# Performance work log

Hardware: AMD Instinct MI355X
Metric: run time of the kernel (lower is better)

Reference implementation:

```python
import jax, jax.numpy as jnp
import numpy as np

B, T, H, V = 32, 16, 768, 32000
EPS = 1e-5


def _conv(x, w, stride, pad):
    return jax.lax.conv_general_dilated(
        x, w, (stride, stride), [(pad, pad), (pad, pad)],
        dimension_numbers=('NCHW', 'OIHW', 'NCHW'))


def _bn(x, g, b, m, v):
    inv = g / jnp.sqrt(v + EPS)
    return x * inv[None, :, None, None] + (b - m * inv)[None, :, None, None]


def setup_inputs() -> dict:
    key = jax.random.key(0)
    ks = iter(jax.random.split(key, 48))

    def rn(shape, s=0.02):
        return s * jax.random.normal(next(ks), shape, jnp.float32)

    def bn_params(c):
        g = 1.0 + 0.1 * jax.random.normal(next(ks), (c,), jnp.float32)
        b = 0.1 * jax.random.normal(next(ks), (c,), jnp.float32)
        m = 0.1 * jax.random.normal(next(ks), (c,), jnp.float32)
        v = jax.random.uniform(next(ks), (c,), jnp.float32, 0.5, 1.5)
        return g, b, m, v

    inp = {}
    inp['images'] = jax.random.normal(next(ks), (B, 3, 224, 224), jnp.float32)
    inp['captions'] = jax.random.randint(next(ks), (B, T), 0, V)

    inp['conv1_w'] = rn((64, 3, 7, 7))
    inp['bn1_g'], inp['bn1_b'], inp['bn1_m'], inp['bn1_v'] = bn_params(64)
    inp['conv2_w'] = rn((128, 64, 3, 3))
    inp['bn2_g'], inp['bn2_b'], inp['bn2_m'], inp['bn2_v'] = bn_params(128)
    inp['conv3_w'] = rn((256, 128, 3, 3))
    inp['bn3_g'], inp['bn3_b'], inp['bn3_m'], inp['bn3_v'] = bn_params(256)
    inp['conv4_w'] = rn((H, 256, 3, 3))
    inp['bn4_g'], inp['bn4_b'], inp['bn4_m'], inp['bn4_v'] = bn_params(H)

    emb = rn((V, H), 1.0)
    inp['emb_table'] = emb.at[0].set(0.0)  # padding_idx=0 row is zero
    inp['attn_w'] = rn((H, H))             # attn_proj (no bias)
    inp['w_ih'] = rn((4 * H, 2 * H))       # LSTM input weights (i,f,g,o)
    inp['w_hh'] = rn((4 * H, H))
    inp['b_ih'] = rn((4 * H,))
    inp['b_hh'] = rn((4 * H,))
    inp['fc_w'] = rn((V, H))
    inp['fc_b'] = rn((V,))
    return inp


def _forward(images, captions, conv1_w, bn1_g, bn1_b, bn1_m, bn1_v,
             conv2_w, bn2_g, bn2_b, bn2_m, bn2_v,
             conv3_w, bn3_g, bn3_b, bn3_m, bn3_v,
             conv4_w, bn4_g, bn4_b, bn4_m, bn4_v,
             emb_table, attn_w, w_ih, w_hh, b_ih, b_hh, fc_w, fc_b):
    # ---- ResNetEncoder ----
    x = jax.nn.relu(_bn(_conv(images, conv1_w, 2, 3), bn1_g, bn1_b, bn1_m, bn1_v))
    x = jax.lax.reduce_window(x, -jnp.inf, jax.lax.max, (1, 1, 3, 3), (1, 1, 2, 2),
                              ((0, 0), (0, 0), (1, 1), (1, 1)))
    x = jax.nn.relu(_bn(_conv(x, conv2_w, 1, 1), bn2_g, bn2_b, bn2_m, bn2_v))
    x = jax.nn.relu(_bn(_conv(x, conv3_w, 2, 1), bn3_g, bn3_b, bn3_m, bn3_v))
    x = jax.nn.relu(_bn(_conv(x, conv4_w, 1, 1), bn4_g, bn4_b, bn4_m, bn4_v))
    b, c, hh, ww = x.shape
    memory = x.reshape(b, c, hh * ww).transpose(0, 2, 1)[:, :196, :]  # [B,196,H]

    # ---- LSTMAttnDecoder ----
    emb = emb_table[captions]  # [B,T,H]
    h0 = jnp.zeros((b, H), jnp.float32)
    c0 = jnp.zeros((b, H), jnp.float32)

    def step(carry, e_t):
        h, cst = carry
        q = h @ attn_w.T                                    # [B,H]
        scores = jnp.einsum('bh,bmh->bm', q, memory)        # [B,196]
        ctx = jnp.einsum('bm,bmh->bh', jax.nn.softmax(scores, axis=-1), memory)
        xin = jnp.concatenate([e_t, ctx], axis=-1)          # [B,2H]
        gates = xin @ w_ih.T + b_ih + h @ w_hh.T + b_hh     # [B,4H]
        i, f, g, o = jnp.split(gates, 4, axis=-1)
        c_new = jax.nn.sigmoid(f) * cst + jax.nn.sigmoid(i) * jnp.tanh(g)
        h_new = jax.nn.sigmoid(o) * jnp.tanh(c_new)
        logits = h_new @ fc_w.T + fc_b                      # [B,V]
        return (h_new, c_new), logits

    (hT, cT), logits = jax.lax.scan(step, (h0, c0), emb.transpose(1, 0, 2))
    logits = logits.transpose(1, 0, 2)  # [B,T,V]
    return logits, (hT[None], cT[None])


def reference(images, captions, conv1_w, bn1_g, bn1_b, bn1_m, bn1_v,
              conv2_w, bn2_g, bn2_b, bn2_m, bn2_v,
              conv3_w, bn3_g, bn3_b, bn3_m, bn3_v,
              conv4_w, bn4_g, bn4_b, bn4_m, bn4_v,
              emb_table, attn_w, w_ih, w_hh, b_ih, b_hh, fc_w, fc_b):
    return _forward(images, captions, conv1_w, bn1_g, bn1_b, bn1_m, bn1_v,
                    conv2_w, bn2_g, bn2_b, bn2_m, bn2_v,
                    conv3_w, bn3_g, bn3_b, bn3_m, bn3_v,
                    conv4_w, bn4_g, bn4_b, bn4_m, bn4_v,
                    emb_table, attn_w, w_ih, w_hh, b_ih, b_hh, fc_w, fc_b)
```

## Files before the change

### kernel.cpp

```cpp
#include <hip/hip_runtime.h>
#include <math.h>

#define NB 32
#define NT 16
#define NH 768
#define NV 32000

typedef short bf16x8 __attribute__((ext_vector_type(8)));
typedef float floatx4 __attribute__((ext_vector_type(4)));
typedef unsigned short ushort_t;

__device__ __forceinline__ float bf2f(unsigned short h) {
    unsigned u = ((unsigned)h) << 16;
    return __builtin_bit_cast(float, u);
}
__device__ __forceinline__ unsigned short f2bf(float f) {
    unsigned u = __builtin_bit_cast(unsigned, f);
    u += 0x7fffu + ((u >> 16) & 1u);
    return (unsigned short)(u >> 16);
}
__device__ __forceinline__ float sigmoidf_(float x) { return 1.f / (1.f + expf(-x)); }

__device__ __forceinline__ int swz8(int bid, int N) {
    return (bid & 7) * (N >> 3) + (bid >> 3);
}

__device__ __forceinline__ bf16x8 cvt8(float4 a, float4 b) {
    bf16x8 t;
    t[0] = (short)f2bf(a.x); t[1] = (short)f2bf(a.y);
    t[2] = (short)f2bf(a.z); t[3] = (short)f2bf(a.w);
    t[4] = (short)f2bf(b.x); t[5] = (short)f2bf(b.y);
    t[6] = (short)f2bf(b.z); t[7] = (short)f2bf(b.w);
    return t;
}

#define SEG0 1216
#define SEG1 (SEG0 + 10240)
#define SEG2 (SEG1 + 73728)
#define SEG3 (SEG2 + 294912)
#define SEG4 (SEG3 + 1769472)
#define SEG5 (SEG4 + 589824)
#define SEG6 (SEG5 + 4718592)
#define SEG7 (SEG6 + 294912)
#define SEG8 (SEG7 + 393216)
#define SEG9 (SEG8 + 49152)
__global__ __launch_bounds__(256) void prep_all(
    const float* __restrict__ g1, const float* __restrict__ b1, const float* __restrict__ m1, const float* __restrict__ v1,
    const float* __restrict__ g2, const float* __restrict__ b2, const float* __restrict__ m2, const float* __restrict__ v2,
    const float* __restrict__ g3, const float* __restrict__ b3, const float* __restrict__ m3, const float* __restrict__ v3,
    const float* __restrict__ g4, const float* __restrict__ b4, const float* __restrict__ m4, const float* __restrict__ v4,
    float* __restrict__ s1, float* __restrict__ o1, float* __restrict__ s2, float* __restrict__ o2,
    float* __restrict__ s3, float* __restrict__ o3, float* __restrict__ s4, float* __restrict__ o4,
    const float* __restrict__ conv1_w, ushort_t* __restrict__ wb1,
    const float* __restrict__ conv2_w, ushort_t* __restrict__ wb2,
    const float* __restrict__ conv3_w, ushort_t* __restrict__ wb3,
    const float* __restrict__ conv4_w, ushort_t* __restrict__ wb4,
    const float* __restrict__ attn_w, ushort_t* __restrict__ wattnTP,
    const float* __restrict__ w_ih, const float* __restrict__ w_hh, ushort_t* __restrict__ wcombP,
    ushort_t* __restrict__ wihL,
    const int* __restrict__ caps, const float* __restrict__ table, ushort_t* __restrict__ e512P,
    float* __restrict__ hbuf, float* __restrict__ cbuf, ushort_t* __restrict__ xinA,
    unsigned long long* __restrict__ halo, long long n8) {
    long long gi = (long long)blockIdx.x * 256 + threadIdx.x;
    if (gi < SEG0) {
        int i = (int)gi;
        const float *g, *b, *m, *v;
        float *s, *o;
        int c;
        if (i < 64)        { g = g1; b = b1; m = m1; v = v1; s = s1; o = o1; c = i; }
        else if (i < 192)  { g = g2; b = b2; m = m2; v = v2; s = s2; o = o2; c = i - 64; }
        else if (i < 448)  { g = g3; b = b3; m = m3; v = v3; s = s3; o = o3; c = i - 192; }
        else               { g = g4; b = b4; m = m4; v = v4; s = s4; o = o4; c = i - 448; }
        float inv = g[c] * rsqrtf(v[c] + 1e-5f);
        s[c] = inv;
        o[c] = b[c] - m[c] * inv;
    } else if (gi < SEG1) {
        int idx = (int)(gi - SEG0);
        int co = idx / 160, k = idx % 160;
        wb1[idx] = (k < 147) ? f2bf(conv1_w[co * 147 + k]) : (ushort_t)0;
    } else if (gi < SEG4) {
        const float* w;
        ushort_t* dst;
        int CIN, idx;
        if (gi < SEG2)      { w = conv2_w; dst = wb2; CIN = 64;  idx = (int)(gi - SEG1); }
        else if (gi < SEG3) { w = conv3_w; dst = wb3; CIN = 128; idx = (int)(gi - SEG2); }
        else                { w = conv4_w; dst = wb4; CIN = 256; idx = (int)(gi - SEG3); }
        int e = idx & 7, lane = (idx >> 3) & 63, j = (idx >> 9) & 3;
        int r = idx >> 11;
        int KQ = CIN >> 5;
        int kq = r % KQ; r /= KQ;
        int tap = r % 9; int nt = r / 9;
        int co = nt * 64 + j * 16 + (lane & 15);
        int ci = kq * 32 + (lane >> 4) * 8 + e;
        dst[idx] = f2bf(w[((size_t)co * CIN + ci) * 9 + tap]);
    } else if (gi < SEG5) {
        int idx = (int)(gi - SEG4);
        int e = idx & 7, lane = (idx >> 3) & 63, j = (idx >> 9) & 3;
        int t = idx >> 11;
        int kq = t % 24, nt = t / 24;
        int n = nt * 64 + 16 * j + (lane & 15);
        int k = kq * 32 + (lane >> 4) * 8 + e;
        wattnTP[idx] = f2bf(attn_w[(size_t)k * 768 + n]);
    } else if (gi < SEG6) {
        int idx = (int)(gi - SEG5);
        int e = idx & 7, lane = (idx >> 3) & 63;
        int t = idx >> 9;
        int kq = t % 48, gg = t / 48;
        int g = gg & 3, bx = gg >> 2;
        int j = g * 768 + bx * 16 + (lane & 15);
        int k = kq * 32 + (lane >> 4) * 8 + e;
        float v = (k < NH) ? w_ih[(size_t)j * (2 * NH) + NH + k] : w_hh[(size_t)j * NH + (k - NH)];
        wcombP[idx] = f2bf(v);
    } else if (gi < SEG7) {
        int idx = (int)(gi - SEG6);
        int r = idx / 96, g = idx % 96;
        const float4* s = (const float4*)(w_ih + (size_t)r * 1536 + g * 8);
        *(bf16x8*)(wihL + (size_t)idx * 8) = cvt8(s[0], s[1]);
    } else if (gi < SEG8) {
        int idx = (int)(gi - SEG7);
        int e = idx & 7, lane = (idx >> 3) & 63, i = (idx >> 9) & 3;
        int t2 = idx >> 11;
        int kq = t2 % 24, mt = t2 / 24;
        int r = mt * 64 + i * 16 + (lane & 15);
        int k = kq * 32 + (lane >> 4) * 8 + e;
        int t = r >> 5, b = r & 31;
        e512P[idx] = f2bf(table[(size_t)caps[b * NT + t] * NH + k]);
    } else if (gi < SEG9) {
        int i = (int)(gi - SEG8);
        xinA[i] = 0;
        if (i < NB * NH) { hbuf[i] = 0.f; cbuf[i] = 0.f; }
    } else {
        long long j = gi - SEG9;
        if (j < n8) halo[j] = 0ULL;
    }
}

__global__ __launch_bounds__(256) void im2col1(const float* __restrict__ img, ushort_t* __restrict__ A) {
    int idx = blockIdx.x * 256 + threadIdx.x;
    const int total = 121856 * 160;
    if (idx >= total) return;
    int k = idx % 160;
    int m = idx / 160;
    ushort_t v = 0;
    if (k < 147) {
        int b = m / 3808;
        int rm = m % 3808;
        int y = rm / 112, x = rm % 112;
        int ci = k / 49;
        int r = k % 49;
        int ky = r / 7, kx = r % 7;
        int iy = 2 * y - 3 + ky;
        int ix = 2 * x - 3 + kx;
        if ((unsigned)iy < 224u && (unsigned)ix < 224u)
            v = f2bf(img[((size_t)(b * 3 + ci) * 224 + iy) * 224 + ix]);
    }
    A[idx] = v;
}

__global__ __launch_bounds__(256) void cvt_b16rows(const float* __restrict__ src, ushort_t* __restrict__ dst,
                                                   int cols8, int ldsrc, int total8) {
    int i = blockIdx.x * 256 + threadIdx.x;
    if (i >= total8) return;
    int r = i / cols8, g = i % cols8;
    const float4* s = (const float4*)(src + (size_t)r * ldsrc + g * 8);
    *(bf16x8*)(dst + (size_t)i * 8) = cvt8(s[0], s[1]);
}

__global__ __launch_bounds__(256) void conv1_gemm(
    const ushort_t* __restrict__ A, const ushort_t* __restrict__ Bw,
    const float* __restrict__ scale, const float* __restrict__ bias,
    ushort_t* __restrict__ out) {
    int lane = threadIdx.x & 63, w = threadIdx.x >> 6;
    int m0 = (blockIdx.x * 4 + w) * 64;
    int lr = lane & 15, kl = (lane >> 4) * 8;
    floatx4 acc[4][4];
    #pragma unroll
    for (int i = 0; i < 4; ++i)
        #pragma unroll
        for (int j = 0; j < 4; ++j) acc[i][j] = 0.f;
    #pragma unroll
    for (int k0 = 0; k0 < 160; k0 += 32) {
        bf16x8 a[4], bb[4];
        #pragma unroll
        for (int i = 0; i < 4; ++i) a[i] = *(const bf16x8*)(A + (size_t)(m0 + 16 * i + lr) * 160 + kl + k0);
        #pragma unroll
        for (int j = 0; j < 4; ++j) bb[j] = *(const bf16x8*)(Bw + (size_t)(16 * j + lr) * 160 + kl + k0);
        #pragma unroll
        for (int i = 0; i < 4; ++i)
            #pragma unroll
            for (int j = 0; j < 4; ++j)
                acc[i][j] = __builtin_amdgcn_mfma_f32_16x16x32_bf16(a[i], bb[j], acc[i][j], 0, 0, 0);
    }
    #pragma unroll
    for (int i = 0; i < 4; ++i) {
        #pragma unroll
        for (int r = 0; r < 4; ++r) {
            int m = m0 + 16 * i + (lane >> 4) * 4 + r;
            int b = m / 3808;
            int rm = m % 3808;
            int y = rm / 112, x = rm % 112;
            #pragma unroll
            for (int j = 0; j < 4; ++j) {
                int n = 16 * j + lr;
                float v = fmaxf(acc[i][j][r] * scale[n] + bias[n], 0.f);
                out[((size_t)(b * 34 + y) * 112 + x) * 64 + n] = f2bf(v);
            }
        }
    }
}

__global__ __launch_bounds__(256) void pool_kernel(const ushort_t* __restrict__ in,
                                                   ushort_t* __restrict__ hal2) {
    int idx = blockIdx.x * 256 + threadIdx.x;
    const int total = 32 * 17 * 56 * 8;
    if (idx >= total) return;
    int c8 = idx & 7;
    int rest = idx >> 3;
    int x = rest % 56; rest /= 56;
    int y = rest % 17; int b = rest / 17;
    float mx[8];
    #pragma unroll
    for (int j = 0; j < 8; ++j) mx[j] = -INFINITY;
    for (int dy = -1; dy <= 1; ++dy) {
        int iy = 2 * y + dy;
        if ((unsigned)iy >= 34u) continue;
        for (int dx = -1; dx <= 1; ++dx) {
            int ix = 2 * x + dx;
            if ((unsigned)ix >= 112u) continue;
            bf16x8 v = *(const bf16x8*)(in + (((size_t)(b * 34 + iy)) * 112 + ix) * 64 + c8 * 8);
            #pragma unroll
            for (int j = 0; j < 8; ++j) mx[j] = fmaxf(mx[j], bf2f((unsigned short)v[j]));
        }
    }
    bf16x8 o;
    #pragma unroll
    for (int j = 0; j < 8; ++j) o[j] = (short)f2bf(mx[j]);
    *(bf16x8*)(hal2 + (((size_t)(b * 19 + y + 1)) * 58 + (x + 1)) * 64 + c8 * 8) = o;
}

template <int CIN, int HH, int WH, int STRIDE, int HOUT, int WOUT, int COUT, int OH, int OW>
__global__ __launch_bounds__(64) void conv_mfma(
    const ushort_t* __restrict__ in, const ushort_t* __restrict__ wtP,
    const float* __restrict__ scale, const float* __restrict__ bias,
    ushort_t* __restrict__ out) {
    const int KQ = CIN / 32;
    const int NK = 9 * KQ;
    const int MT = (32 * HOUT * WOUT) / 64;
    const int NTL = COUT / 64;
    int id = swz8(blockIdx.x, MT * NTL);
    int mt = id % MT, nt = id / MT;
    int lane = threadIdx.x;
    int lr = lane & 15, kl = (lane >> 4) * 8;
    int rowoff[4];
    #pragma unroll
    for (int i = 0; i < 4; ++i) {
        int m = mt * 64 + 16 * i + lr;
        int b = m / (HOUT * WOUT);
        int rm = m % (HOUT * WOUT);
        int y = rm / WOUT, x = rm % WOUT;
        rowoff[i] = ((b * HH + y * STRIDE) * WH + x * STRIDE) * CIN + kl;
    }
    floatx4 acc[4][4];
    #pragma unroll
    for (int i = 0; i < 4; ++i)
        #pragma unroll
        for (int j = 0; j < 4; ++j) acc[i][j] = 0.f;

    auto ioffOf = [&](int ks) {
        int tap = ks / KQ;
        int k0 = (ks & (KQ - 1)) * 32;
        int ky = tap / 3, kx = tap - ky * 3;
        return (ky * WH + kx) * CIN + k0;
    };
    const ushort_t* bbase = wtP + ((size_t)nt * 9 * KQ * 4 * 64 + lane) * 8;

    bf16x8 aC[4], bC[4], aN[4], bN[4];
    {
        int io = ioffOf(0);
        #pragma unroll
        for (int i = 0; i < 4; ++i) aC[i] = *(const bf16x8*)(in + rowoff[i] + io);
        #pragma unroll
        for (int j = 0; j < 4; ++j) bC[j] = *(const bf16x8*)(bbase + ((size_t)j * 64) * 8);
    }
    for (int ks = 0; ks < NK; ks += 2) {
        {
            int io = ioffOf(ks + 1);
            #pragma unroll
            for (int i = 0; i < 4; ++i) aN[i] = *(const bf16x8*)(in + rowoff[i] + io);
            #pragma unroll
            for (int j = 0; j < 4; ++j) bN[j] = *(const bf16x8*)(bbase + ((size_t)((ks + 1) * 4 + j) * 64) * 8);
        }
        #pragma unroll
        for (int i = 0; i < 4; ++i)
            #pragma unroll
            for (int j = 0; j < 4; ++j)
                acc[i][j] = __builtin_amdgcn_mfma_f32_16x16x32_bf16(aC[i], bC[j], acc[i][j], 0, 0, 0);
        if (ks + 2 < NK) {
            int io = ioffOf(ks + 2);
            #pragma unroll
            for (int i = 0; i < 4; ++i) aC[i] = *(const bf16x8*)(in + rowoff[i] + io);
            #pragma unroll
            for (int j = 0; j < 4; ++j) bC[j] = *(const bf16x8*)(bbase + ((size_t)((ks + 2) * 4 + j) * 64) * 8);
        }
        #pragma unroll
        for (int i = 0; i < 4; ++i)
            #pragma unroll
            for (int j = 0; j < 4; ++j)
                acc[i][j] = __builtin_amdgcn_mfma_f32_16x16x32_bf16(aN[i], bN[j], acc[i][j], 0, 0, 0);
    }
    #pragma unroll
    for (int i = 0; i < 4; ++i) {
        #pragma unroll
        for (int r = 0; r < 4; ++r) {
            int m = mt * 64 + 16 * i + (lane >> 4) * 4 + r;
            int b = m / (HOUT * WOUT);
            int rm = m % (HOUT * WOUT);
            int y = rm / WOUT, x = rm % WOUT;
            #pragma unroll
            for (int j = 0; j < 4; ++j) {
                int n = nt * 64 + 16 * j + lr;
                float v = fmaxf(acc[i][j][r] * scale[n] + bias[n], 0.f);
                out[((size_t)(b * OH + y + 1) * OW + (x + 1)) * COUT + n] = f2bf(v);
            }
        }
    }
}

__global__ __launch_bounds__(64) void conv4_split(
    const ushort_t* __restrict__ in, const ushort_t* __restrict__ wtP,
    float* __restrict__ part) {
    const int CIN = 256, HH = 10, WH = 30, HOUT = 7, WOUT = 28;
    int id = swz8(blockIdx.x, 98 * 12 * 3);
    int s = id / (98 * 12);
    int rem = id % (98 * 12);
    int nt = rem / 98, mt = rem % 98;
    int lane = threadIdx.x;
    int lr = lane & 15, kl = (lane >> 4) * 8;
    int rowoff[4];
    #pragma unroll
    for (int i = 0; i < 4; ++i) {
        int m = mt * 64 + 16 * i + lr;
        int b = m / (HOUT * WOUT);
        int rm = m % (HOUT * WOUT);
        int y = rm / WOUT, x = rm % WOUT;
        rowoff[i] = ((b * HH + y) * WH + x) * CIN + kl;
    }
    floatx4 acc[4][4];
    #pragma unroll
    for (int i = 0; i < 4; ++i)
        #pragma unroll
        for (int j = 0; j < 4; ++j) acc[i][j] = 0.f;

    auto ioffOf = [&](int ks) {
        int tap = s * 3 + (ks >> 3);
        int k0 = (ks & 7) * 32;
        int ky = tap / 3, kx = tap - ky * 3;
        return (ky * WH + kx) * CIN + k0;
    };
    const ushort_t* bbase = wtP + ((size_t)nt * 9 * 8 * 4 * 64 + lane) * 8;
    auto bOf = [&](int ks, int j) {
        return (const bf16x8*)(bbase + ((size_t)((s * 24 + ks) * 4 + j) * 64) * 8);
    };

    bf16x8 aC[4], bC[4], aN[4], bN[4];
    {
        int io = ioffOf(0);
        #pragma unroll
        for (int i = 0; i < 4; ++i) aC[i] = *(const bf16x8*)(in + rowoff[i] + io);
        #pragma unroll
        for (int j = 0; j < 4; ++j) bC[j] = *bOf(0, j);
    }
    for (int ks = 0; ks < 24; ks += 2) {
        {
            int io = ioffOf(ks + 1);
            #pragma unroll
            for (int i = 0; i < 4; ++i) aN[i] = *(const bf16x8*)(in + rowoff[i] + io);
            #pragma unroll
            for (int j = 0; j < 4; ++j) bN[j] = *bOf(ks + 1, j);
        }
        #pragma unroll
        for (int i = 0; i < 4; ++i)
            #pragma unroll
            for (int j = 0; j < 4; ++j)
                acc[i][j] = __builtin_amdgcn_mfma_f32_16x16x32_bf16(aC[i], bC[j], acc[i][j], 0, 0, 0);
        if (ks + 2 < 24) {
            int io = ioffOf(ks + 2);
            #pragma unroll
            for (int i = 0; i < 4; ++i) aC[i] = *(const bf16x8*)(in + rowoff[i] + io);
            #pragma unroll
            for (int j = 0; j < 4; ++j) bC[j] = *bOf(ks + 2, j);
        }
        #pragma unroll
        for (int i = 0; i < 4; ++i)
            #pragma unroll
            for (int j = 0; j < 4; ++j)
                acc[i][j] = __builtin_amdgcn_mfma_f32_16x16x32_bf16(aN[i], bN[j], acc[i][j], 0, 0, 0);
    }
    float* pbase = part + (size_t)s * 6272 * 768;
    #pragma unroll
    for (int i = 0; i < 4; ++i) {
        #pragma unroll
        for (int r = 0; r < 4; ++r) {
            int m = mt * 64 + 16 * i + (lane >> 4) * 4 + r;
            #pragma unroll
            for (int j = 0; j < 4; ++j) {
                int n = nt * 64 + 16 * j + lr;
                pbase[(size_t)m * 768 + n] = acc[i][j][r];
            }
        }
    }
}

__global__ __launch_bounds__(256) void comb4(
    const float* __restrict__ part, const float* __restrict__ scale, const float* __restrict__ bias,
    ushort_t* __restrict__ memv) {
    int idx = blockIdx.x * 256 + threadIdx.x;
    if (idx >= 6272 * 192) return;
    int m = idx / 192, nq = idx % 192;
    int n = nq * 4;
    size_t off = (size_t)m * 768 + n;
    const float4 a = *(const float4*)(part + off);
    const float4 b = *(const float4*)(part + (size_t)6272 * 768 + off);
    const float4 c = *(const float4*)(part + (size_t)2 * 6272 * 768 + off);
    ushort_t o[4];
    o[0] = f2bf(fmaxf((a.x + b.x + c.x) * scale[n]     + bias[n],     0.f));
    o[1] = f2bf(fmaxf((a.y + b.y + c.y) * scale[n + 1] + bias[n + 1], 0.f));
    o[2] = f2bf(fmaxf((a.z + b.z + c.z) * scale[n + 2] + bias[n + 2], 0.f));
    o[3] = f2bf(fmaxf((a.w + b.w + c.w) * scale[n + 3] + bias[n + 3], 0.f));
    *(unsigned long long*)(memv + off) = *(unsigned long long*)o;
}

__global__ __launch_bounds__(64) void kmat_gemm(
    const ushort_t* __restrict__ memv, const ushort_t* __restrict__ Bp,
    ushort_t* __restrict__ KT) {
    int id = swz8(blockIdx.x, 98 * 12);
    int mt = id % 98, nt = id / 98;
    int lane = threadIdx.x;
    int lr = lane & 15, kl = (lane >> 4) * 8;
    const ushort_t* arow[4];
    #pragma unroll
    for (int i = 0; i < 4; ++i) arow[i] = memv + (size_t)(mt * 64 + 16 * i + lr) * 768 + kl;
    const ushort_t* bbase = Bp + ((size_t)nt * 24 * 4 * 64 + lane) * 8;
    floatx4 acc[4][4];
    #pragma unroll
    for (int i = 0; i < 4; ++i)
        #pragma unroll
        for (int j = 0; j < 4; ++j) acc[i][j] = 0.f;
    bf16x8 aC[4], bC[4], aN[4], bN[4];
    #pragma unroll
    for (int i = 0; i < 4; ++i) aC[i] = *(const bf16x8*)(arow[i]);
    #pragma unroll
    for (int j = 0; j < 4; ++j) bC[j] = *(const bf16x8*)(bbase + ((size_t)j * 64) * 8);
    for (int ks = 0; ks < 24; ks += 2) {
        #pragma unroll
        for (int i = 0; i < 4; ++i) aN[i] = *(const bf16x8*)(arow[i] + (ks + 1) * 32);
        #pragma unroll
        for (int j = 0; j < 4; ++j) bN[j] = *(const bf16x8*)(bbase + ((size_t)((ks + 1) * 4 + j) * 64) * 8);
        #pragma unroll
        for (int i = 0; i < 4; ++i)
            #pragma unroll
            for (int j = 0; j < 4; ++j)
                acc[i][j] = __builtin_amdgcn_mfma_f32_16x16x32_bf16(aC[i], bC[j], acc[i][j], 0, 0, 0);
        if (ks + 2 < 24) {
            #pragma unroll
            for (int i = 0; i < 4; ++i) aC[i] = *(const bf16x8*)(arow[i] + (ks + 2) * 32);
            #pragma unroll
            for (int j = 0; j < 4; ++j) bC[j] = *(const bf16x8*)(bbase + ((size_t)((ks + 2) * 4 + j) * 64) * 8);
        }
        #pragma unroll
        for (int i = 0; i < 4; ++i)
            #pragma unroll
            for (int j = 0; j < 4; ++j)
                acc[i][j] = __builtin_amdgcn_mfma_f32_16x16x32_bf16(aN[i], bN[j], acc[i][j], 0, 0, 0);
    }
    #pragma unroll
    for (int i = 0; i < 4; ++i) {
        #pragma unroll
        for (int r = 0; r < 4; ++r) {
            int mg = mt * 64 + 16 * i + (lane >> 4) * 4 + r;
            int b = mg / 196, m = mg % 196;
            #pragma unroll
            for (int j = 0; j < 4; ++j) {
                int n = nt * 64 + 16 * j + lr;
                KT[(((size_t)b * 96 + (n >> 3)) * 196 + m) * 8 + (n & 7)] = f2bf(acc[i][j][r]);
            }
        }
    }
}

template <int REMAP>
__global__ __launch_bounds__(256, 4) void gemm_ldsb(
    const ushort_t* __restrict__ Ap, const ushort_t* __restrict__ Bb,
    const float* __restrict__ bias1, const float* __restrict__ bias2,
    float* __restrict__ C, int N) {
    __shared__ ushort_t bt[2][64 * 72];
    int tid = threadIdx.x;
    int lane = tid & 63, w = tid >> 6;
    int nblk = (N >> 6) * 2;
    int id = swz8(blockIdx.x, nblk);
    int nt = id >> 1, mh = id & 1;
    int n0 = nt * 64;
    int mt = mh * 4 + w;
    int lr = lane & 15, hi = lane >> 4;
    int srow = tid >> 2, sc = tid & 3;
    const ushort_t* gsrc = Bb + (size_t)(n0 + srow) * 768 + sc * 8;
    int woff = srow * 72 + sc * 8;
    floatx4 acc[4][4];
    #pragma unroll
    for (int i = 0; i < 4; ++i)
        #pragma unroll
        for (int j = 0; j < 4; ++j) acc[i][j] = 0.f;
    bf16x8 s0 = *(const bf16x8*)(gsrc);
    bf16x8 s1 = *(const bf16x8*)(gsrc + 32);
    for (int kc = 0; kc < 12; ++kc) {
        ushort_t* bufw = &bt[kc & 1][0];
        *(bf16x8*)(bufw + woff) = s0;
        *(bf16x8*)(bufw + woff + 32) = s1;
        if (kc < 11) {
            const ushort_t* p = gsrc + (size_t)(kc + 1) * 64;
            s0 = *(const bf16x8*)(p);
            s1 = *(const bf16x8*)(p + 32);
        }
        __syncthreads();
        const ushort_t* bufr = &bt[kc & 1][0];
        #pragma unroll
        for (int kk = 0; kk < 2; ++kk) {
            int kq = kc * 2 + kk;
            bf16x8 bfr[4], a[4];
            #pragma unroll
            for (int j = 0; j < 4; ++j)
                bfr[j] = *(const bf16x8*)(bufr + (j * 16 + lr) * 72 + kk * 32 + hi * 8);
            #pragma unroll
            for (int i = 0; i < 4; ++i)
                a[i] = *(const bf16x8*)(Ap + ((((size_t)mt * 24 + kq) * 4 + i) * 64 + lane) * 8);
            #pragma unroll
            for (int i = 0; i < 4; ++i)
                #pragma unroll
                for (int j = 0; j < 4; ++j)
                    acc[i][j] = __builtin_amdgcn_mfma_f32_16x16x32_bf16(a[i], bfr[j], acc[i][j], 0, 0, 0);
        }
    }
    #pragma unroll
    for (int i = 0; i < 4; ++i) {
        #pragma unroll
        for (int rr = 0; rr < 4; ++rr) {
            int m = mt * 64 + 16 * i + hi * 4 + rr;
            #pragma unroll
            for (int j = 0; j < 4; ++j) {
                int n = n0 + 16 * j + lr;
                float vv = acc[i][j][rr];
                if (bias1) vv += bias1[n];
                if (bias2) vv += bias2[n];
                if (REMAP) {
                    int t = m >> 5, b = m & 31;
                    C[(size_t)((b << 4) + t) * NV + n] = vv;
                } else {
                    C[(size_t)m * N + n] = vv;
                }
            }
        }
    }
}

__global__ __launch_bounds__(768) void attn2(
    ushort_t* __restrict__ xin, const ushort_t* __restrict__ KT,
    const ushort_t* __restrict__ mem) {
    __shared__ float hq[NH];
    __shared__ float sl[196];
    __shared__ float red[16];
    int b = blockIdx.x, tid = threadIdx.x;
    hq[tid] = bf2f(xin[(size_t)b * 1536 + NH + tid]);
    __syncthreads();
    if (tid < 392) {
        int m = tid >> 1, half = tid & 1;
        const ushort_t* basep = KT + (((size_t)b * 96 + half * 48) * 196 + m) * 8;
        float acc = 0.f;
        #pragma unroll 4
        for (int k8 = 0; k8 < 48; ++k8) {
            bf16x8 v = *(const bf16x8*)(basep + (size_t)k8 * 196 * 8);
            const float* qp = hq + (half * 48 + k8) * 8;
            #pragma unroll
            for (int j = 0; j < 8; ++j)
                acc = fmaf(bf2f((unsigned short)v[j]), qp[j], acc);
        }
        acc += __shfl_xor(acc, 1);
        if (!half) sl[m] = acc;
    }
    __syncthreads();
    float sc = (tid < 196) ? sl[tid] : -INFINITY;
    float v = sc;
    #pragma unroll
    for (int off = 32; off; off >>= 1) v = fmaxf(v, __shfl_down(v, off));
    if ((tid & 63) == 0) red[tid >> 6] = v;
    __syncthreads();
    if (tid == 0) {
        float m = red[0];
        for (int i = 1; i < 12; ++i) m = fmaxf(m, red[i]);
        red[12] = m;
    }
    __syncthreads();
    float mx = red[12];
    float e = (tid < 196) ? expf(sc - mx) : 0.f;
    __syncthreads();
    v = e;
    #pragma unroll
    for (int off = 32; off; off >>= 1) v += __shfl_down(v, off);
    if ((tid & 63) == 0) red[tid >> 6] = v;
    __syncthreads();
    if (tid == 0) {
        float s = red[0];
        for (int i = 1; i < 12; ++i) s += red[i];
        red[12] = 1.f / s;
    }
    __syncthreads();
    if (tid < 196) sl[tid] = e * red[12];
    __syncthreads();
    {
        float acc = 0.f;
        const ushort_t* mb = mem + (size_t)b * 196 * NH + tid;
        #pragma unroll 4
        for (int m = 0; m < 196; ++m) acc = fmaf(sl[m], bf2f(mb[(size_t)m * NH]), acc);
        xin[(size_t)b * 1536 + tid] = f2bf(acc);
    }
}

__global__ __launch_bounds__(256) void step_fused(
    const ushort_t* __restrict__ xin_r, const ushort_t* __restrict__ wcombP,
    const float* __restrict__ eg_t,
    float* __restrict__ cbuf, float* __restrict__ hbuf,
    ushort_t* __restrict__ xin_w, ushort_t* __restrict__ hallP, int tstep) {
    __shared__ float pbuf[4][64][33];
    int lane = threadIdx.x & 63, w = threadIdx.x >> 6;
    int bx = blockIdx.x;
    int lr = lane & 15, kl = (lane >> 4) * 8;
    floatx4 acc[2][4];
    #pragma unroll
    for (int i = 0; i < 2; ++i)
        #pragma unroll
        for (int g = 0; g < 4; ++g) acc[i][g] = 0.f;
    for (int kq = 0; kq < 12; ++kq) {
        int k = w * 384 + kq * 32;
        bf16x8 a[2], bb[4];
        #pragma unroll
        for (int i = 0; i < 2; ++i)
            a[i] = *(const bf16x8*)(xin_r + (size_t)(16 * i + lr) * 1536 + k + kl);
        #pragma unroll
        for (int g = 0; g < 4; ++g)
            bb[g] = *(const bf16x8*)(wcombP + (((size_t)(bx * 4 + g) * 48 + (w * 12 + kq)) * 64 + lane) * 8);
        #pragma unroll
        for (int i = 0; i < 2; ++i)
            #pragma unroll
            for (int g = 0; g < 4; ++g)
                acc[i][g] = __builtin_amdgcn_mfma_f32_16x16x32_bf16(a[i], bb[g], acc[i][g], 0, 0, 0);
    }
    #pragma unroll
    for (int i = 0; i < 2; ++i)
        #pragma unroll
        for (int g = 0; g < 4; ++g)
            #pragma unroll
            for (int r = 0; r < 4; ++r) {
                int m = 16 * i + (lane >> 4) * 4 + r;
                pbuf[w][g * 16 + lr][m] = acc[i][g][r];
            }
    __syncthreads();
    int tid = threadIdx.x;
    #pragma unroll
    for (int o = 0; o < 2; ++o) {
        int pid = tid * 2 + o;
        int m = pid & 31, c = pid >> 5;
        int kcol = bx * 16 + c;
        float gi = 0.f, gf = 0.f, gg = 0.f, go = 0.f;
        #pragma unroll
        for (int ww = 0; ww < 4; ++ww) {
            gi += pbuf[ww][c][m];
            gf += pbuf[ww][16 + c][m];
            gg += pbuf[ww][32 + c][m];
            go += pbuf[ww][48 + c][m];
        }
        const float* eg = eg_t + (size_t)m * 3072;
        gi += eg[kcol];
        gf += eg[768 + kcol];
        gg += eg[1536 + kcol];
        go += eg[2304 + kcol];
        float cst = cbuf[m * 768 + kcol];
        float cn = sigmoidf_(gf) * cst + sigmoidf_(gi) * tanhf(gg);
        float hn = sigmoidf_(go) * tanhf(cn);
        cbuf[m * 768 + kcol] = cn;
        hbuf[m * 768 + kcol] = hn;
        ushort_t hb = f2bf(hn);
        xin_w[(size_t)m * 1536 + NH + kcol] = hb;
        int rrow = tstep * 32 + m;
        int mtp = rrow >> 6, ip = (rrow >> 4) & 3, lrp = rrow & 15;
        int kqp = kcol >> 5, hip = (kcol >> 3) & 3, ep = kcol & 7;
        hallP[((((size_t)mtp * 24 + kqp) * 4 + ip) * 64 + (lrp | (hip << 4))) * 8 + ep] = hb;
    }
}

__global__ __launch_bounds__(256) void copy_hc(const float* __restrict__ h, const float* __restrict__ c,
                                               float* __restrict__ out) {
    int i = blockIdx.x * 256 + threadIdx.x;
    if (i < NB * NH) {
        out[(size_t)NB * NT * NV + i] = h[i];
        out[(size_t)NB * NT * NV + NB * NH + i] = c[i];
    }
}

extern "C" void kernel_launch(void* const* d_in, const int* in_sizes, int n_in,
                              void* d_out, int out_size, void* d_ws, size_t ws_size,
                              hipStream_t stream) {
    const float* images   = (const float*)d_in[0];
    const int*   captions = (const int*)d_in[1];
    const float* conv1_w  = (const float*)d_in[2];
    const float* bn1_g = (const float*)d_in[3], *bn1_b = (const float*)d_in[4];
    const float* bn1_m = (const float*)d_in[5], *bn1_v = (const float*)d_in[6];
    const float* conv2_w  = (const float*)d_in[7];
    const float* bn2_g = (const float*)d_in[8], *bn2_b = (const float*)d_in[9];
    const float* bn2_m = (const float*)d_in[10], *bn2_v = (const float*)d_in[11];
    const float* conv3_w  = (const float*)d_in[12];
    const float* bn3_g = (const float*)d_in[13], *bn3_b = (const float*)d_in[14];
    const float* bn3_m = (const float*)d_in[15], *bn3_v = (const float*)d_in[16];
    const float* conv4_w  = (const float*)d_in[17];
    const float* bn4_g = (const float*)d_in[18], *bn4_b = (const float*)d_in[19];
    const float* bn4_m = (const float*)d_in[20], *bn4_v = (const float*)d_in[21];
    const float* emb_table = (const float*)d_in[22];
    const float* attn_w   = (const float*)d_in[23];
    const float* w_ih     = (const float*)d_in[24];
    const float* w_hh     = (const float*)d_in[25];
    const float* b_ih     = (const float*)d_in[26];
    const float* b_hh     = (const float*)d_in[27];
    const float* fc_w     = (const float*)d_in[28];
    const float* fc_b     = (const float*)d_in[29];
    float* out = (float*)d_out;

    char* base = (char*)d_ws;
    size_t off = 0;
    auto alloc = [&](size_t bytes) { char* p = base + off; off += (bytes + 255) & ~(size_t)255; return p; };
    float* s1 = (float*)alloc(64 * 4);   float* bb1 = (float*)alloc(64 * 4);
    float* s2 = (float*)alloc(128 * 4);  float* bb2 = (float*)alloc(128 * 4);
    float* s3 = (float*)alloc(256 * 4);  float* bb3 = (float*)alloc(256 * 4);
    float* s4 = (float*)alloc(768 * 4);  float* bb4 = (float*)alloc(768 * 4);
    ushort_t* c1out = (ushort_t*)alloc((size_t)32 * 34 * 112 * 64 * 2);
    size_t halo_start = off;
    ushort_t* hal2 = (ushort_t*)alloc((size_t)32 * 19 * 58 * 64 * 2);
    ushort_t* hal3 = (ushort_t*)alloc((size_t)32 * 18 * 58 * 128 * 2);
    ushort_t* hal4 = (ushort_t*)alloc((size_t)32 * 10 * 30 * 256 * 2);
    size_t halo_bytes = off - halo_start;
    ushort_t* memv = (ushort_t*)alloc((size_t)32 * 196 * 768 * 2);
    ushort_t* KT   = (ushort_t*)alloc((size_t)32 * 96 * 196 * 8 * 2);
    ushort_t* wb1 = (ushort_t*)alloc((size_t)64 * 160 * 2);
    ushort_t* wb2 = (ushort_t*)alloc((size_t)128 * 9 * 64 * 2);
    ushort_t* wb3 = (ushort_t*)alloc((size_t)256 * 9 * 128 * 2);
    ushort_t* wb4 = (ushort_t*)alloc((size_t)768 * 9 * 256 * 2);
    ushort_t* wattnTP = (ushort_t*)alloc((size_t)768 * 768 * 2);
    ushort_t* wcombP = (ushort_t*)alloc((size_t)3072 * 1536 * 2);
    ushort_t* wihL = (ushort_t*)alloc((size_t)3072 * 768 * 2);
    ushort_t* e512P = (ushort_t*)alloc((size_t)512 * 768 * 2);
    float* eg   = (float*)alloc((size_t)512 * 3072 * 4);
    ushort_t* HallP = (ushort_t*)alloc((size_t)512 * 768 * 2);
    float* hbuf = (float*)alloc(NB * NH * 4);
    float* cbuf = (float*)alloc(NB * NH * 4);
    ushort_t* xinA = (ushort_t*)alloc((size_t)NB * 1536 * 2);
    ushort_t* xinB = (ushort_t*)alloc((size_t)NB * 1536 * 2);
    float* part = (float*)alloc((size_t)3 * 6272 * 768 * 4);
    char* ubig = alloc((size_t)NV * NH * 2);
    ushort_t* imcol = (ushort_t*)ubig;
    ushort_t* fcwb  = (ushort_t*)ubig;

    long long n8 = (long long)(halo_bytes / 8);
    long long prep_total = (long long)SEG9 + n8;
    prep_all<<<(unsigned)((prep_total + 255) / 256), 256, 0, stream>>>(
        bn1_g, bn1_b, bn1_m, bn1_v, bn2_g, bn2_b, bn2_m, bn2_v,
        bn3_g, bn3_b, bn3_m, bn3_v, bn4_g, bn4_b, bn4_m, bn4_v,
        s1, bb1, s2, bb2, s3, bb3, s4, bb4,
        conv1_w, wb1, conv2_w, wb2, conv3_w, wb3, conv4_w, wb4,
        attn_w, wattnTP, w_ih, w_hh, wcombP, wihL,
        captions, emb_table, e512P,
        hbuf, cbuf, xinA,
        (unsigned long long*)hal2, n8);

    gemm_ldsb<0><<<96, 256, 0, stream>>>(e512P, wihL, b_ih, b_hh, eg, 3072);

    im2col1<<<(121856 * 160 + 255) / 256, 256, 0, stream>>>(images, imcol);
    conv1_gemm<<<476, 256, 0, stream>>>(imcol, wb1, s1, bb1, c1out);
    cvt_b16rows<<<(NV * 96 + 255) / 256, 256, 0, stream>>>(fc_w, fcwb, 96, 768, NV * 96);
    pool_kernel<<<(32 * 17 * 56 * 8 + 255) / 256, 256, 0, stream>>>(c1out, hal2);
    conv_mfma<64, 19, 58, 1, 16, 56, 128, 18, 58>
        <<<896, 64, 0, stream>>>(hal2, wb2, s2, bb2, hal3);
    conv_mfma<128, 18, 58, 2, 8, 28, 256, 10, 30>
        <<<448, 64, 0, stream>>>(hal3, wb3, s3, bb3, hal4);
    conv4_split<<<3528, 64, 0, stream>>>(hal4, wb4, part);
    comb4<<<(6272 * 192 + 255) / 256, 256, 0, stream>>>(part, s4, bb4, memv);

    kmat_gemm<<<1176, 64, 0, stream>>>(memv, wattnTP, KT);

    ushort_t* xcur = xinA;
    ushort_t* xnxt = xinB;
    for (int t = 0; t < NT; ++t) {
        attn2<<<NB, NH, 0, stream>>>(xcur, KT, memv);
        step_fused<<<48, 256, 0, stream>>>(
            xcur, wcombP, eg + (size_t)t * NB * 3072, cbuf, hbuf, xnxt, HallP, t);
        ushort_t* tmp = xcur; xcur = xnxt; xnxt = tmp;
    }

    gemm_ldsb<1><<<1000, 256, 0, stream>>>(HallP, fcwb, fc_b, nullptr, out, NV);

    copy_hc<<<(NB * NH + 255) / 256, 256, 0, stream>>>(hbuf, cbuf, out);
}
```

Measured before the change: 902.4 us.

## Share A tiles across four waves via LDS in conv4 and kmat GEMMs

Conv4 no longer splits K three ways into fp32 partials plus a combine kernel. It now runs 256-thread blocks where four waves, each covering a different N tile, share one double-buffered LDS copy of the A tile, and BN+ReLU is applied in the epilogue. The attention key GEMM gets the same LDS sharing scheme. This removes the partial buffer traffic, one launch and redundant A loads, but drops the grid from 3528 blocks to 294. It also adds two barriers per K step, which may cost latency hiding and occupancy.

```diff
diff --git a/kernel.cpp b/kernel.cpp
--- a/kernel.cpp
+++ b/kernel.cpp
@@ -326,25 +326,25 @@
     }
 }
 
-__global__ __launch_bounds__(64) void conv4_split(
+__global__ __launch_bounds__(256) void conv4_lds(
     const ushort_t* __restrict__ in, const ushort_t* __restrict__ wtP,
-    float* __restrict__ part) {
-    const int CIN = 256, HH = 10, WH = 30, HOUT = 7, WOUT = 28;
-    int id = swz8(blockIdx.x, 98 * 12 * 3);
-    int s = id / (98 * 12);
-    int rem = id % (98 * 12);
-    int nt = rem / 98, mt = rem % 98;
-    int lane = threadIdx.x;
+    const float* __restrict__ scale, const float* __restrict__ bias,
+    ushort_t* __restrict__ memv) {
+    const int CIN = 256, WH = 30, HOUT = 7, WOUT = 28;
+    __shared__ ushort_t at[2][64 * 40];
+    int tid = threadIdx.x;
+    int lane = tid & 63, w = tid >> 6;
+    int mt = blockIdx.x;
+    int nt = blockIdx.y * 4 + w;
     int lr = lane & 15, kl = (lane >> 4) * 8;
-    int rowoff[4];
-    #pragma unroll
-    for (int i = 0; i < 4; ++i) {
-        int m = mt * 64 + 16 * i + lr;
-        int b = m / (HOUT * WOUT);
-        int rm = m % (HOUT * WOUT);
-        int y = rm / WOUT, x = rm % WOUT;
-        rowoff[i] = ((b * HH + y) * WH + x) * CIN + kl;
-    }
+    int srow = tid >> 2, sc = tid & 3;
+    int m_s = mt * 64 + srow;
+    int b_s = m_s / 196, rm_s = m_s % 196;
+    int y_s = rm_s / 28, x_s = rm_s % 28;
+    const ushort_t* arow = in + ((size_t)(b_s * 10 + y_s) * 30 + x_s) * CIN + sc * 8;
+    ushort_t* wslot = &at[0][0];
+    int woff = srow * 40 + sc * 8;
+
     floatx4 acc[4][4];
     #pragma unroll
     for (int i = 0; i < 4; ++i)
@@ -352,51 +352,32 @@
         for (int j = 0; j < 4; ++j) acc[i][j] = 0.f;
 
     auto ioffOf = [&](int ks) {
-        int tap = s * 3 + (ks >> 3);
+        int tap = ks >> 3;
         int k0 = (ks & 7) * 32;
         int ky = tap / 3, kx = tap - ky * 3;
         return (ky * WH + kx) * CIN + k0;
     };
-    const ushort_t* bbase = wtP + ((size_t)nt * 9 * 8 * 4 * 64 + lane) * 8;
-    auto bOf = [&](int ks, int j) {
-        return (const bf16x8*)(bbase + ((size_t)((s * 24 + ks) * 4 + j) * 64) * 8);
-    };
-
-    bf16x8 aC[4], bC[4], aN[4], bN[4];
-    {
-        int io = ioffOf(0);
-        #pragma unroll
-        for (int i = 0; i < 4; ++i) aC[i] = *(const bf16x8*)(in + rowoff[i] + io);
-        #pragma unroll
-        for (int j = 0; j < 4; ++j) bC[j] = *bOf(0, j);
-    }
-    for (int ks = 0; ks < 24; ks += 2) {
-        {
-            int io = ioffOf(ks + 1);
-            #pragma unroll
-            for (int i = 0; i < 4; ++i) aN[i] = *(const bf16x8*)(in + rowoff[i] + io);
-            #pragma unroll
-            for (int j = 0; j < 4; ++j) bN[j] = *bOf(ks + 1, j);
-        }
+    const ushort_t* bbase = wtP + ((size_t)nt * 72 * 4 * 64 + lane) * 8;
+
+    bf16x8 sreg = *(const bf16x8*)(arow + ioffOf(0));
+    for (int ks = 0; ks < 72; ++ks) {
+        *(bf16x8*)(&at[ks & 1][0] + woff) = sreg;
+        if (ks + 1 < 72) sreg = *(const bf16x8*)(arow + ioffOf(ks + 1));
+        __syncthreads();
+        bf16x8 a[4], bb[4];
+        #pragma unroll
+        for (int j = 0; j < 4; ++j)
+            bb[j] = *(const bf16x8*)(bbase + ((size_t)(ks * 4 + j) * 64) * 8);
         #pragma unroll
         for (int i = 0; i < 4; ++i)
+            a[i] = *(const bf16x8*)(&at[ks & 1][0] + (16 * i + lr) * 40 + kl);
+        #pragma unroll
+        for (int i = 0; i < 4; ++i)
             #pragma unroll
             for (int j = 0; j < 4; ++j)
-                acc[i][j] = __builtin_amdgcn_mfma_f32_16x16x32_bf16(aC[i], bC[j], acc[i][j], 0, 0, 0);
-        if (ks + 2 < 24) {
-            int io = ioffOf(ks + 2);
-            #pragma unroll
-            for (int i = 0; i < 4; ++i) aC[i] = *(const bf16x8*)(in + rowoff[i] + io);
-            #pragma unroll
-            for (int j = 0; j < 4; ++j) bC[j] = *bOf(ks + 2, j);
-        }
-        #pragma unroll
-        for (int i = 0; i < 4; ++i)
-            #pragma unroll
-            for (int j = 0; j < 4; ++j)
-                acc[i][j] = __builtin_amdgcn_mfma_f32_16x16x32_bf16(aN[i], bN[j], acc[i][j], 0, 0, 0);
-    }
-    float* pbase = part + (size_t)s * 6272 * 768;
+                acc[i][j] = __builtin_amdgcn_mfma_f32_16x16x32_bf16(a[i], bb[j], acc[i][j], 0, 0, 0);
+        __syncthreads();
+    }
     #pragma unroll
     for (int i = 0; i < 4; ++i) {
         #pragma unroll
@@ -405,73 +386,51 @@
             #pragma unroll
             for (int j = 0; j < 4; ++j) {
                 int n = nt * 64 + 16 * j + lr;
-                pbase[(size_t)m * 768 + n] = acc[i][j][r];
+                float v = fmaxf(acc[i][j][r] * scale[n] + bias[n], 0.f);
+                memv[(size_t)m * 768 + n] = f2bf(v);
             }
         }
     }
 }
 
-__global__ __launch_bounds__(256) void comb4(
-    const float* __restrict__ part, const float* __restrict__ scale, const float* __restrict__ bias,
-    ushort_t* __restrict__ memv) {
-    int idx = blockIdx.x * 256 + threadIdx.x;
-    if (idx >= 6272 * 192) return;
-    int m = idx / 192, nq = idx % 192;
-    int n = nq * 4;
-    size_t off = (size_t)m * 768 + n;
-    const float4 a = *(const float4*)(part + off);
-    const float4 b = *(const float4*)(part + (size_t)6272 * 768 + off);
-    const float4 c = *(const float4*)(part + (size_t)2 * 6272 * 768 + off);
-    ushort_t o[4];
-    o[0] = f2bf(fmaxf((a.x + b.x + c.x) * scale[n]     + bias[n],     0.f));
-    o[1] = f2bf(fmaxf((a.y + b.y + c.y) * scale[n + 1] + bias[n + 1], 0.f));
-    o[2] = f2bf(fmaxf((a.z + b.z + c.z) * scale[n + 2] + bias[n + 2], 0.f));
-    o[3] = f2bf(fmaxf((a.w + b.w + c.w) * scale[n + 3] + bias[n + 3], 0.f));
-    *(unsigned long long*)(memv + off) = *(unsigned long long*)o;
-}
-
-__global__ __launch_bounds__(64) void kmat_gemm(
+__global__ __launch_bounds__(256) void kmat_lds(
     const ushort_t* __restrict__ memv, const ushort_t* __restrict__ Bp,
     ushort_t* __restrict__ KT) {
-    int id = swz8(blockIdx.x, 98 * 12);
-    int mt = id % 98, nt = id / 98;
-    int lane = threadIdx.x;
+    __shared__ ushort_t at[2][64 * 40];
+    int tid = threadIdx.x;
+    int lane = tid & 63, w = tid >> 6;
+    int mt = blockIdx.x;
+    int nt = blockIdx.y * 4 + w;
     int lr = lane & 15, kl = (lane >> 4) * 8;
-    const ushort_t* arow[4];
-    #pragma unroll
-    for (int i = 0; i < 4; ++i) arow[i] = memv + (size_t)(mt * 64 + 16 * i + lr) * 768 + kl;
+    int srow = tid >> 2, sc = tid & 3;
+    const ushort_t* arow = memv + (size_t)(mt * 64 + srow) * 768 + sc * 8;
+    int woff = srow * 40 + sc * 8;
     const ushort_t* bbase = Bp + ((size_t)nt * 24 * 4 * 64 + lane) * 8;
+
     floatx4 acc[4][4];
     #pragma unroll
     for (int i = 0; i < 4; ++i)
         #pragma unroll
         for (int j = 0; j < 4; ++j) acc[i][j] = 0.f;
-    bf16x8 aC[4], bC[4], aN[4], bN[4];
-    #pragma unroll
-    for (int i = 0; i < 4; ++i) aC[i] = *(const bf16x8*)(arow[i]);
-    #pragma unroll
-    for (int j = 0; j < 4; ++j) bC[j] = *(const bf16x8*)(bbase + ((size_t)j * 64) * 8);
-    for (int ks = 0; ks < 24; ks += 2) {
-        #pragma unroll
-        for (int i = 0; i < 4; ++i) aN[i] = *(const bf16x8*)(arow[i] + (ks + 1) * 32);
-        #pragma unroll
-        for (int j = 0; j < 4; ++j) bN[j] = *(const bf16x8*)(bbase + ((size_t)((ks + 1) * 4 + j) * 64) * 8);
+
+    bf16x8 sreg = *(const bf16x8*)(arow);
+    for (int ks = 0; ks < 24; ++ks) {
+        *(bf16x8*)(&at[ks & 1][0] + woff) = sreg;
+        if (ks + 1 < 24) sreg = *(const bf16x8*)(arow + (ks + 1) * 32);
+        __syncthreads();
+        bf16x8 a[4], bb[4];
+        #pragma unroll
+        for (int j = 0; j < 4; ++j)
+            bb[j] = *(const bf16x8*)(bbase + ((size_t)(ks * 4 + j) * 64) * 8);
         #pragma unroll
         for (int i = 0; i < 4; ++i)
+            a[i] = *(const bf16x8*)(&at[ks & 1][0] + (16 * i + lr) * 40 + kl);
+        #pragma unroll
+        for (int i = 0; i < 4; ++i)
             #pragma unroll
             for (int j = 0; j < 4; ++j)
-                acc[i][j] = __builtin_amdgcn_mfma_f32_16x16x32_bf16(aC[i], bC[j], acc[i][j], 0, 0, 0);
-        if (ks + 2 < 24) {
-            #pragma unroll
-            for (int i = 0; i < 4; ++i) aC[i] = *(const bf16x8*)(arow[i] + (ks + 2) * 32);
-            #pragma unroll
-            for (int j = 0; j < 4; ++j) bC[j] = *(const bf16x8*)(bbase + ((size_t)((ks + 2) * 4 + j) * 64) * 8);
-        }
-        #pragma unroll
-        for (int i = 0; i < 4; ++i)
-            #pragma unroll
-            for (int j = 0; j < 4; ++j)
-                acc[i][j] = __builtin_amdgcn_mfma_f32_16x16x32_bf16(aN[i], bN[j], acc[i][j], 0, 0, 0);
+                acc[i][j] = __builtin_amdgcn_mfma_f32_16x16x32_bf16(a[i], bb[j], acc[i][j], 0, 0, 0);
+        __syncthreads();
     }
     #pragma unroll
     for (int i = 0; i < 4; ++i) {
@@ -761,7 +720,6 @@
     float* cbuf = (float*)alloc(NB * NH * 4);
     ushort_t* xinA = (ushort_t*)alloc((size_t)NB * 1536 * 2);
     ushort_t* xinB = (ushort_t*)alloc((size_t)NB * 1536 * 2);
-    float* part = (float*)alloc((size_t)3 * 6272 * 768 * 4);
     char* ubig = alloc((size_t)NV * NH * 2);
     ushort_t* imcol = (ushort_t*)ubig;
     ushort_t* fcwb  = (ushort_t*)ubig;
@@ -788,10 +746,9 @@
         <<<896, 64, 0, stream>>>(hal2, wb2, s2, bb2, hal3);
     conv_mfma<128, 18, 58, 2, 8, 28, 256, 10, 30>
         <<<448, 64, 0, stream>>>(hal3, wb3, s3, bb3, hal4);
-    conv4_split<<<3528, 64, 0, stream>>>(hal4, wb4, part);
-    comb4<<<(6272 * 192 + 255) / 256, 256, 0, stream>>>(part, s4, bb4, memv);
-
-    kmat_gemm<<<1176, 64, 0, stream>>>(memv, wattnTP, KT);
+    conv4_lds<<<dim3(98, 3), 256, 0, stream>>>(hal4, wb4, s4, bb4, memv);
+
+    kmat_lds<<<dim3(98, 3), 256, 0, stream>>>(memv, wattnTP, KT);
 
     ushort_t* xcur = xinA;
     ushort_t* xnxt = xinB;
```

After: 880.0 us. 1.03x faster.
